# Performance work log

Measured on AMD Instinct MI355X. Metric: run time of the kernel, lower is better.

Reference implementation:

```python
import jax, jax.numpy as jnp
import numpy as np

NUM_INPUTS = 256
NUM_OUTPUTS = 256
NUM_MID_LAYERS = 15  # num_layers=16 -> 1 first + 15 middle + 1 output layer
N = 16384            # num_neurons_per_layer
W = 4096             # bitarray width (parallel evaluations)


def setup_inputs() -> dict:
    key = jax.random.key(0)
    k0, k1, k2, k3, k4, k5, k6 = jax.random.split(key, 7)
    input_bits = jax.random.randint(k0, (NUM_INPUTS, W), 0, 2).astype(jnp.bool_)
    idx0 = jax.random.randint(k1, (N, 2), 0, NUM_INPUTS, dtype=jnp.int32)
    idx_mid = jax.random.randint(k2, (NUM_MID_LAYERS, N, 2), 0, N, dtype=jnp.int32)
    idx_out = jax.random.randint(k3, (NUM_OUTPUTS, 2), 0, N, dtype=jnp.int32)
    nor0 = jax.random.randint(k4, (N,), 0, 2).astype(jnp.bool_)
    nor_mid = jax.random.randint(k5, (NUM_MID_LAYERS, N), 0, 2).astype(jnp.bool_)
    nor_out = jax.random.randint(k6, (NUM_OUTPUTS,), 0, 2).astype(jnp.bool_)
    return {"input_bits": input_bits, "idx0": idx0, "idx_mid": idx_mid,
            "idx_out": idx_out, "nor0": nor0, "nor_mid": nor_mid, "nor_out": nor_out}


def _nand_layer(x, idx, nor):
    # x: [num_in, W] bool; idx: [num_out, 2]; nor: [num_out]
    a = x[idx[:, 0]]  # [num_out, W]
    b = x[idx[:, 1]]
    # NOT(where(nor, a|b, a&b))  == per-node NOR or NAND
    return ~jnp.where(nor[:, None], a | b, a & b)


def reference(input_bits, idx0, idx_mid, idx_out, nor0, nor_mid, nor_out):
    x = _nand_layer(input_bits, idx0, nor0)  # [N, W]

    def step(x, layer):
        idx, nor = layer
        return _nand_layer(x, idx, nor), None

    x, _ = jax.lax.scan(step, x, (idx_mid, nor_mid))
    out = _nand_layer(x, idx_out, nor_out)  # [NUM_OUTPUTS, W]
    return out
```

## Files before the change

kernel.cpp:

```cpp
#include <hip/hip_runtime.h>
#include <stdint.h>

#define N_GATES    16384
#define NUM_IN     256
#define NUM_OUT    256
#define MID_LAYERS 15
#define W          4096
#define BLOCK      1024
#define WG_COLS    16
#define NUM_WG     (W / WG_COLS)
#define QPT        (N_GATES / (4 * BLOCK))

__global__ __launch_bounds__(BLOCK, 2)
void nand_graph_kernel(const uint32_t* __restrict__ input_bits,
                       const int4*     __restrict__ idx0_4,
                       const int4*     __restrict__ idx_mid_4,
                       const int2*     __restrict__ idx_out,
                       const int4*     __restrict__ nor0_4,
                       const int4*     __restrict__ nor_mid_4,
                       const uint32_t* __restrict__ nor_out,
                       int*            __restrict__ out)
{
    extern __shared__ __align__(16) uint16_t lds16[];
    uint16_t* bufA = lds16;
    uint16_t* bufB = lds16 + N_GATES;
    uint16_t* wrd  = lds16 + 2 * N_GATES;

    const int tid     = threadIdx.x;
    const int lane    = tid & 63;
    const int wave    = tid >> 6;
    const int colbase = blockIdx.x * WG_COLS;

    int4 ixA[QPT], ixB[QPT], nnq[QPT];

    #pragma unroll
    for (int q = 0; q < QPT; ++q) {
        int Q = tid + q * BLOCK;
        ixA[q] = idx0_4[2 * Q];
        ixB[q] = idx0_4[2 * Q + 1];
        nnq[q] = nor0_4[Q];
    }

    #pragma unroll
    for (int it = wave; it < NUM_IN / 4; it += BLOCK / 64) {
        int r = it * 4 + (lane >> 4);
        int c = lane & 15;
        uint32_t v = input_bits[r * W + colbase + c];
        unsigned long long m = __ballot(v != 0u);
        if ((lane & 15) == 0)
            wrd[r] = (uint16_t)(m >> ((lane >> 4) * 16));
    }
    __syncthreads();

    auto run_gates = [&](const uint16_t* __restrict__ src, uint16_t* __restrict__ dst) {
        #pragma unroll
        for (int q = 0; q < QPT; ++q) {
            int Q = tid + q * BLOCK;
            uint32_t a0 = src[ixA[q].x], b0 = src[ixA[q].y];
            uint32_t a1 = src[ixA[q].z], b1 = src[ixA[q].w];
            uint32_t a2 = src[ixB[q].x], b2 = src[ixB[q].y];
            uint32_t a3 = src[ixB[q].z], b3 = src[ixB[q].w];
            uint32_t r0 = ~(nnq[q].x ? (a0 | b0) : (a0 & b0));
            uint32_t r1 = ~(nnq[q].y ? (a1 | b1) : (a1 & b1));
            uint32_t r2 = ~(nnq[q].z ? (a2 | b2) : (a2 & b2));
            uint32_t r3 = ~(nnq[q].w ? (a3 | b3) : (a3 & b3));
            uint32_t lo = (r0 & 0xFFFFu) | (r1 << 16);
            uint32_t hi = (r2 & 0xFFFFu) | (r3 << 16);
            *reinterpret_cast<uint2*>(dst + 4 * Q) = make_uint2(lo, hi);
        }
    };

    run_gates(wrd, bufA);
    {
        const int4* i4 = idx_mid_4;
        const int4* n4 = nor_mid_4;
        #pragma unroll
        for (int q = 0; q < QPT; ++q) {
            int Q = tid + q * BLOCK;
            ixA[q] = i4[2 * Q];
            ixB[q] = i4[2 * Q + 1];
            nnq[q] = n4[Q];
        }
    }
    __syncthreads();

    uint16_t* cur = bufA;
    uint16_t* nxt = bufB;
    for (int l = 0; l < MID_LAYERS; ++l) {
        run_gates(cur, nxt);
        if (l + 1 < MID_LAYERS) {
            const int4* i4 = idx_mid_4 + (size_t)(l + 1) * (N_GATES / 2);
            const int4* n4 = nor_mid_4 + (size_t)(l + 1) * (N_GATES / 4);
            #pragma unroll
            for (int q = 0; q < QPT; ++q) {
                int Q = tid + q * BLOCK;
                ixA[q] = i4[2 * Q];
                ixB[q] = i4[2 * Q + 1];
                nnq[q] = n4[Q];
            }
        }
        __syncthreads();
        uint16_t* t = cur; cur = nxt; nxt = t;
    }

    if (tid < NUM_OUT) {
        int2 ix = idx_out[tid];
        uint32_t a = cur[ix.x];
        uint32_t b = cur[ix.y];
        wrd[tid] = (uint16_t)~(nor_out[tid] ? (a | b) : (a & b));
    }
    __syncthreads();

    #pragma unroll
    for (int i = tid; i < NUM_OUT * WG_COLS; i += BLOCK) {
        int r = i >> 4, c = i & 15;
        out[r * W + colbase + c] = (int)((wrd[r] >> c) & 1u);
    }
}

extern "C" void kernel_launch(void* const* d_in, const int* in_sizes, int n_in,
                              void* d_out, int out_size, void* d_ws, size_t ws_size,
                              hipStream_t stream) {
    const uint32_t* input_bits = (const uint32_t*)d_in[0];
    const int4*     idx0_4     = (const int4*)d_in[1];
    const int4*     idx_mid_4  = (const int4*)d_in[2];
    const int2*     idx_out    = (const int2*)d_in[3];
    const int4*     nor0_4     = (const int4*)d_in[4];
    const int4*     nor_mid_4  = (const int4*)d_in[5];
    const uint32_t* nor_out    = (const uint32_t*)d_in[6];
    int*            out        = (int*)d_out;

    const size_t lds_bytes = (size_t)(2 * N_GATES + 256) * sizeof(uint16_t);

    hipFuncSetAttribute(reinterpret_cast<const void*>(nand_graph_kernel),
                        hipFuncAttributeMaxDynamicSharedMemorySize, (int)lds_bytes);

    nand_graph_kernel<<<dim3(NUM_WG), dim3(BLOCK), lds_bytes, stream>>>(
        input_bits, idx0_4, idx_mid_4, idx_out, nor0_4, nor_mid_4, nor_out, out);
}
```

Before: 43.73 us.

## Precompute packed, bank-conflict-aware gate descriptors in a prep kernel

```diff
diff --git a/kernel.cpp b/kernel.cpp
--- a/kernel.cpp
+++ b/kernel.cpp
@@ -5,11 +5,149 @@
 #define NUM_IN     256
 #define NUM_OUT    256
 #define MID_LAYERS 15
+#define LAYERS_TOT 16
 #define W          4096
 #define BLOCK      1024
 #define WG_COLS    16
 #define NUM_WG     (W / WG_COLS)
-#define QPT        (N_GATES / (4 * BLOCK))
+#define QPT        4
+
+__global__ __launch_bounds__(64)
+void prep_sched(const int2* __restrict__ idx0,
+                const int*  __restrict__ nor0,
+                const int2* __restrict__ idx_mid,
+                const int*  __restrict__ nor_mid,
+                uint32_t*   __restrict__ ws)
+{
+    __shared__ uint32_t desc_s[1024];
+    __shared__ uint32_t binsA[32 * 16];
+    __shared__ uint32_t binsB[32 * 16];
+
+    const int l = blockIdx.x >> 4;
+    const int w = blockIdx.x & 15;
+    const int t = threadIdx.x;
+
+    const int2* idx = (l == 0) ? idx0 : idx_mid + (size_t)(l - 1) * N_GATES;
+    const int*  nor = (l == 0) ? nor0 : nor_mid + (size_t)(l - 1) * N_GATES;
+
+    for (int j = t; j < 1024; j += 64) {
+        int q = j >> 8, i = j & 255;
+        int g = w * 256 + q * 4096 + i;
+        int2 ab = idx[g];
+        int  nn = nor[g];
+        desc_s[j] = (uint32_t)ab.x | ((uint32_t)ab.y << 14) | ((uint32_t)nn << 28);
+    }
+    for (int j = t; j < 32 * 16; j += 64) { binsA[j] = 0; binsB[j] = 0; }
+    __syncthreads();
+
+    if (t < 16) {
+        const int q = t >> 2, k = t & 3;
+        for (int lane = 0; lane < 64; ++lane) {
+            uint32_t d = desc_s[q * 256 + lane * 4 + k];
+            uint32_t a = d & 0x3FFFu, b = (d >> 14) & 0x3FFFu, n = d >> 28;
+            uint32_t ba = (a >> 1) & 31, bb = (b >> 1) & 31;
+            uint32_t laa = binsA[ba * 16 + t], lbb = binsB[bb * 16 + t];
+            uint32_t lab = binsA[bb * 16 + t], lba = binsB[ba * 16 + t];
+            uint32_t c0 = laa > lbb ? laa : lbb;
+            uint32_t c1 = lab > lba ? lab : lba;
+            uint32_t s0 = a, s1 = b, nA = laa, nB = lbb;
+            if (c1 < c0) { s0 = b; s1 = a; nA = lab; nB = lba; }
+            binsA[((s0 >> 1) & 31) * 16 + t] = nA + 1;
+            binsB[((s1 >> 1) & 31) * 16 + t] = nB + 1;
+            uint32_t Q = (uint32_t)(w * 64 + lane + q * 1024);
+            ws[(size_t)l * N_GATES + Q * 4 + k] = (s0 << 1) | (n << 15) | (s1 << 17);
+        }
+    }
+}
+
+__global__ __launch_bounds__(BLOCK, 2)
+void nand_graph_sched(const uint32_t* __restrict__ input_bits,
+                      const uint32_t* __restrict__ ws_desc,
+                      const int2*     __restrict__ idx_out,
+                      const uint32_t* __restrict__ nor_out,
+                      int*            __restrict__ out)
+{
+    extern __shared__ __align__(16) uint16_t lds16[];
+    uint16_t* bufA = lds16;
+    uint16_t* bufB = lds16 + N_GATES;
+    uint16_t* wrd  = lds16 + 2 * N_GATES;
+
+    const int tid     = threadIdx.x;
+    const int lane    = tid & 63;
+    const int wave    = tid >> 6;
+    const int colbase = blockIdx.x * WG_COLS;
+    const uint4* dsc4 = reinterpret_cast<const uint4*>(ws_desc);
+
+    uint4 dsc[QPT];
+    #pragma unroll
+    for (int q = 0; q < QPT; ++q)
+        dsc[q] = dsc4[q * 1024 + tid];
+
+    #pragma unroll
+    for (int it = wave; it < NUM_IN / 4; it += BLOCK / 64) {
+        int r = it * 4 + (lane >> 4);
+        int c = lane & 15;
+        uint32_t v = input_bits[r * W + colbase + c];
+        unsigned long long m = __ballot(v != 0u);
+        if ((lane & 15) == 0)
+            wrd[r] = (uint16_t)(m >> ((lane >> 4) * 16));
+    }
+    __syncthreads();
+
+    auto gate = [](const uint16_t* __restrict__ src, uint32_t d) -> uint32_t {
+        uint32_t a2 = d & 0x7FFEu;
+        uint32_t b2 = d >> 16;
+        uint32_t va = *(const uint16_t*)((const char*)src + a2);
+        uint32_t vb = *(const uint16_t*)((const char*)src + b2);
+        return ~((d & 0x8000u) ? (va | vb) : (va & vb));
+    };
+
+    auto run_gates = [&](const uint16_t* __restrict__ src, uint16_t* __restrict__ dst) {
+        #pragma unroll
+        for (int q = 0; q < QPT; ++q) {
+            int Q = tid + q * BLOCK;
+            uint32_t r0 = gate(src, dsc[q].x);
+            uint32_t r1 = gate(src, dsc[q].y);
+            uint32_t r2 = gate(src, dsc[q].z);
+            uint32_t r3 = gate(src, dsc[q].w);
+            uint32_t lo = (r0 & 0xFFFFu) | (r1 << 16);
+            uint32_t hi = (r2 & 0xFFFFu) | (r3 << 16);
+            *reinterpret_cast<uint2*>(dst + 4 * Q) = make_uint2(lo, hi);
+        }
+    };
+
+    run_gates(wrd, bufA);
+    #pragma unroll
+    for (int q = 0; q < QPT; ++q)
+        dsc[q] = dsc4[1 * 4096 + q * 1024 + tid];
+    __syncthreads();
+
+    uint16_t* cur = bufA;
+    uint16_t* nxt = bufB;
+    for (int l = 1; l <= MID_LAYERS; ++l) {
+        run_gates(cur, nxt);
+        if (l + 1 <= MID_LAYERS) {
+            #pragma unroll
+            for (int q = 0; q < QPT; ++q)
+                dsc[q] = dsc4[(l + 1) * 4096 + q * 1024 + tid];
+        }
+        __syncthreads();
+        uint16_t* tp = cur; cur = nxt; nxt = tp;
+    }
+
+    if (tid < NUM_OUT) {
+        int2 ix = idx_out[tid];
+        uint32_t a = cur[ix.x];
+        uint32_t b = cur[ix.y];
+        wrd[tid] = (uint16_t)~(nor_out[tid] ? (a | b) : (a & b));
+    }
+    __syncthreads();
+
+    for (int i = tid; i < NUM_OUT * WG_COLS; i += BLOCK) {
+        int r = i >> 4, c = i & 15;
+        out[r * W + colbase + c] = (int)((wrd[r] >> c) & 1u);
+    }
+}
 
 __global__ __launch_bounds__(BLOCK, 2)
 void nand_graph_kernel(const uint32_t* __restrict__ input_bits,
@@ -32,7 +170,6 @@
     const int colbase = blockIdx.x * WG_COLS;
 
     int4 ixA[QPT], ixB[QPT], nnq[QPT];
-
     #pragma unroll
     for (int q = 0; q < QPT; ++q) {
         int Q = tid + q * BLOCK;
@@ -40,7 +177,6 @@
         ixB[q] = idx0_4[2 * Q + 1];
         nnq[q] = nor0_4[Q];
     }
-
     #pragma unroll
     for (int it = wave; it < NUM_IN / 4; it += BLOCK / 64) {
         int r = it * 4 + (lane >> 4);
@@ -72,14 +208,12 @@
 
     run_gates(wrd, bufA);
     {
-        const int4* i4 = idx_mid_4;
-        const int4* n4 = nor_mid_4;
         #pragma unroll
         for (int q = 0; q < QPT; ++q) {
             int Q = tid + q * BLOCK;
-            ixA[q] = i4[2 * Q];
-            ixB[q] = i4[2 * Q + 1];
-            nnq[q] = n4[Q];
+            ixA[q] = idx_mid_4[2 * Q];
+            ixB[q] = idx_mid_4[2 * Q + 1];
+            nnq[q] = nor_mid_4[Q];
         }
     }
     __syncthreads();
@@ -100,7 +234,7 @@
             }
         }
         __syncthreads();
-        uint16_t* t = cur; cur = nxt; nxt = t;
+        uint16_t* tp = cur; cur = nxt; nxt = tp;
     }
 
     if (tid < NUM_OUT) {
@@ -110,8 +244,6 @@
         wrd[tid] = (uint16_t)~(nor_out[tid] ? (a | b) : (a & b));
     }
     __syncthreads();
-
-    #pragma unroll
     for (int i = tid; i < NUM_OUT * WG_COLS; i += BLOCK) {
         int r = i >> 4, c = i & 15;
         out[r * W + colbase + c] = (int)((wrd[r] >> c) & 1u);
@@ -122,19 +254,29 @@
                               void* d_out, int out_size, void* d_ws, size_t ws_size,
                               hipStream_t stream) {
     const uint32_t* input_bits = (const uint32_t*)d_in[0];
-    const int4*     idx0_4     = (const int4*)d_in[1];
-    const int4*     idx_mid_4  = (const int4*)d_in[2];
+    const int2*     idx0       = (const int2*)d_in[1];
+    const int2*     idx_mid    = (const int2*)d_in[2];
     const int2*     idx_out    = (const int2*)d_in[3];
-    const int4*     nor0_4     = (const int4*)d_in[4];
-    const int4*     nor_mid_4  = (const int4*)d_in[5];
+    const int*      nor0       = (const int*)d_in[4];
+    const int*      nor_mid    = (const int*)d_in[5];
     const uint32_t* nor_out    = (const uint32_t*)d_in[6];
     int*            out        = (int*)d_out;
 
     const size_t lds_bytes = (size_t)(2 * N_GATES + 256) * sizeof(uint16_t);
-
-    hipFuncSetAttribute(reinterpret_cast<const void*>(nand_graph_kernel),
-                        hipFuncAttributeMaxDynamicSharedMemorySize, (int)lds_bytes);
-
-    nand_graph_kernel<<<dim3(NUM_WG), dim3(BLOCK), lds_bytes, stream>>>(
-        input_bits, idx0_4, idx_mid_4, idx_out, nor0_4, nor_mid_4, nor_out, out);
-}
+    const size_t desc_bytes = (size_t)LAYERS_TOT * N_GATES * sizeof(uint32_t);
+
+    if (ws_size >= desc_bytes) {
+        uint32_t* ws = (uint32_t*)d_ws;
+        prep_sched<<<dim3(256), dim3(64), 0, stream>>>(idx0, nor0, idx_mid, nor_mid, ws);
+        hipFuncSetAttribute(reinterpret_cast<const void*>(nand_graph_sched),
+                            hipFuncAttributeMaxDynamicSharedMemorySize, (int)lds_bytes);
+        nand_graph_sched<<<dim3(NUM_WG), dim3(BLOCK), lds_bytes, stream>>>(
+            input_bits, ws, idx_out, nor_out, out);
+    } else {
+        hipFuncSetAttribute(reinterpret_cast<const void*>(nand_graph_kernel),
+                            hipFuncAttributeMaxDynamicSharedMemorySize, (int)lds_bytes);
+        nand_graph_kernel<<<dim3(NUM_WG), dim3(BLOCK), lds_bytes, stream>>>(
+            input_bits, (const int4*)idx0, (const int4*)idx_mid, idx_out,
+            (const int4*)nor0, (const int4*)nor_mid, nor_out, out);
+    }
+}
```

Result: slower. 51.78 us (+18.4%).
